# Performance work log

Measured on AMD Instinct MI355X. Metric: run time of the kernel, lower is better.

Reference implementation:

```python
import jax, jax.numpy as jnp
import numpy as np

N_NODES = 100000
HIDDEN = 64
N_EDGES = 1600000


def _sage_conv(x, edge_index, Wl, Wr, b):
    # PyG SAGEConv (mean aggr): out_i = W_l @ mean_{j->i} x_j + W_r @ x_i + b
    src, dst = edge_index[0], edge_index[1]
    msg = x[src]                                      # [E, H] gather
    agg = jax.ops.segment_sum(msg, dst, num_segments=N_NODES)  # [N, H]
    deg = jax.ops.segment_sum(jnp.ones((msg.shape[0],), x.dtype), dst,
                              num_segments=N_NODES)
    agg = agg / jnp.maximum(deg, 1.0)[:, None]
    return agg @ Wl.T + x @ Wr.T + b


def setup_inputs() -> dict:
    key = jax.random.key(0)
    ks = jax.random.split(key, 8)
    s = 1.0 / np.sqrt(HIDDEN)
    return {
        "emb": jax.random.normal(ks[0], (N_NODES, HIDDEN), jnp.float32),
        "Wl1": jax.random.normal(ks[1], (HIDDEN, HIDDEN), jnp.float32) * s,
        "Wr1": jax.random.normal(ks[2], (HIDDEN, HIDDEN), jnp.float32) * s,
        "b1": jnp.zeros((HIDDEN,), jnp.float32),
        "Wl2": jax.random.normal(ks[3], (HIDDEN, HIDDEN), jnp.float32) * s,
        "Wr2": jax.random.normal(ks[4], (HIDDEN, HIDDEN), jnp.float32) * s,
        "b2": jnp.zeros((HIDDEN,), jnp.float32),
        "node_id": jnp.arange(N_NODES, dtype=jnp.int64 if jax.config.jax_enable_x64 else jnp.int32),
        "edge_index": jax.random.randint(ks[5], (2, N_EDGES), 0, N_NODES),
    }


def reference(emb, Wl1, Wr1, b1, Wl2, Wr2, b2, node_id, edge_index):
    # Embedding lookup
    x = emb[node_id]                                   # [N, H]
    # GNN: relu(conv1) -> conv2
    x = jax.nn.relu(_sage_conv(x, edge_index, Wl1, Wr1, b1))
    x = _sage_conv(x, edge_index, Wl2, Wr2, b2)
    # Classifier: per-edge dot product of endpoint features
    ef1 = x[edge_index[0]]                             # [E, H]
    ef2 = x[edge_index[1]]                             # [E, H]
    return (ef1 * ef2).sum(axis=-1)                    # [E]
```

## Files before the change

### kernel.cpp

```cpp
#include <hip/hip_runtime.h>

#define N_NODES 100000
#define HID 64
#define N_EDGES 1600000
#define NB 391
#define C_EPB 6400

typedef __attribute__((ext_vector_type(8))) short bf16x8;
typedef __attribute__((ext_vector_type(4))) float f32x4;

__device__ __forceinline__ unsigned short f2bf(float f) {
    unsigned u = __float_as_uint(f);
    u = (u + 0x7FFFu + ((u >> 16) & 1u)) >> 16;
    return (unsigned short)u;
}
__device__ __forceinline__ float bf2f(unsigned short h) {
    return __uint_as_float(((unsigned)h) << 16);
}
__device__ __forceinline__ float bflo(unsigned w) { return __uint_as_float(w << 16); }
__device__ __forceinline__ float bfhi(unsigned w) { return __uint_as_float(w & 0xFFFF0000u); }

__global__ void gather_bf16_kernel(const float* __restrict__ emb,
                                   const int* __restrict__ nid,
                                   unsigned short* __restrict__ xh) {
    int i = blockIdx.x * blockDim.x + threadIdx.x;
    const int total = N_NODES * (HID / 4);
    if (i >= total) return;
    int row = i >> 4;
    int c   = i & 15;
    int s   = nid[row];
    float4 v = reinterpret_cast<const float4*>(emb)[(size_t)s * 16 + c];
    uint2 p;
    p.x = (unsigned)f2bf(v.x) | ((unsigned)f2bf(v.y) << 16);
    p.y = (unsigned)f2bf(v.z) | ((unsigned)f2bf(v.w) << 16);
    reinterpret_cast<uint2*>(xh)[(size_t)row * 16 + c] = p;
}

__global__ void bucket_hist(const int* __restrict__ dst,
                            int* __restrict__ bhist) {
    __shared__ int h[NB];
    for (int i = threadIdx.x; i < NB; i += blockDim.x) h[i] = 0;
    __syncthreads();
    int nt = gridDim.x * blockDim.x;
    const int4* d4 = (const int4*)dst;
    for (int q = blockIdx.x * blockDim.x + threadIdx.x; q < N_EDGES / 4; q += nt) {
        int4 v = d4[q];
        atomicAdd(&h[v.x >> 8], 1);
        atomicAdd(&h[v.y >> 8], 1);
        atomicAdd(&h[v.z >> 8], 1);
        atomicAdd(&h[v.w >> 8], 1);
    }
    __syncthreads();
    for (int i = threadIdx.x; i < NB; i += blockDim.x)
        if (h[i]) atomicAdd(&bhist[i], h[i]);
}

__global__ void bucket_scan(const int* __restrict__ bhist,
                            int* __restrict__ boff,
                            int* __restrict__ bcursor) {
    __shared__ int s[512];
    int v = (threadIdx.x < NB) ? bhist[threadIdx.x] : 0;
    s[threadIdx.x] = v;
    __syncthreads();
    for (int off = 1; off < 512; off <<= 1) {
        int t = (threadIdx.x >= off) ? s[threadIdx.x - off] : 0;
        __syncthreads();
        s[threadIdx.x] += t;
        __syncthreads();
    }
    if (threadIdx.x < NB) {
        int ex = s[threadIdx.x] - v;
        boff[threadIdx.x] = ex;
        bcursor[threadIdx.x] = ex;
    }
}

__global__ void bucket_scatter(const int* __restrict__ src,
                               const int* __restrict__ dst,
                               int* __restrict__ bcursor,
                               int2* __restrict__ pairs) {
    __shared__ int h[NB];
    __shared__ int base[NB];
    for (int i = threadIdx.x; i < NB; i += blockDim.x) h[i] = 0;
    __syncthreads();
    int e0 = blockIdx.x * C_EPB;
    int e1 = e0 + C_EPB; if (e1 > N_EDGES) e1 = N_EDGES;
    for (int e = e0 + threadIdx.x; e < e1; e += blockDim.x)
        atomicAdd(&h[dst[e] >> 8], 1);
    __syncthreads();
    for (int i = threadIdx.x; i < NB; i += blockDim.x) {
        int c = h[i];
        base[i] = c ? atomicAdd(&bcursor[i], c) : 0;
    }
    __syncthreads();
    for (int i = threadIdx.x; i < NB; i += blockDim.x) h[i] = 0;
    __syncthreads();
    for (int e = e0 + threadIdx.x; e < e1; e += blockDim.x) {
        int d = dst[e];
        int b = d >> 8;
        int slot = base[b] + atomicAdd(&h[b], 1);
        pairs[slot] = make_int2(src[e], d);
    }
}

__global__ void bucket_csr(const int2* __restrict__ pairs,
                           const int* __restrict__ boff,
                           const int* __restrict__ bcursor,
                           int* __restrict__ row_start,
                           int* __restrict__ adj) {
    __shared__ int cnt[256];
    __shared__ int sc[256];
    int b = blockIdx.x;
    int node0 = b << 8;
    int p0 = boff[b];
    int p1 = bcursor[b];
    int t = threadIdx.x;
    cnt[t] = 0;
    __syncthreads();
    for (int p = p0 + t; p < p1; p += 256)
        atomicAdd(&cnt[pairs[p].y & 255], 1);
    __syncthreads();
    int v = cnt[t];
    sc[t] = v;
    __syncthreads();
    for (int off = 1; off < 256; off <<= 1) {
        int u = (t >= off) ? sc[t - off] : 0;
        __syncthreads();
        sc[t] += u;
        __syncthreads();
    }
    sc[t] = p0 + sc[t] - v;
    __syncthreads();
    int node = node0 + t;
    if (node <= N_NODES) row_start[node] = sc[t];
    __syncthreads();
    for (int p = p0 + t; p < p1; p += 256) {
        int2 pr = pairs[p];
        int slot = atomicAdd(&sc[pr.y & 255], 1);
        adj[slot] = pr.x;
    }
}

__global__ void agg_kernel(const int* __restrict__ row_start,
                           const int* __restrict__ adj,
                           const unsigned short* __restrict__ xh,
                           unsigned short* __restrict__ M) {
    int lane = threadIdx.x & 63;
    int slot = lane >> 4;
    int c    = lane & 15;
    int wpb = blockDim.x >> 6;
    int wid = blockIdx.x * wpb + (threadIdx.x >> 6);
    int stride = gridDim.x * wpb;
    const uint2* xw = (const uint2*)xh;
    uint2* Mw = (uint2*)M;
    for (int row = wid; row < N_NODES; row += stride) {
        int beg = row_start[row], end = row_start[row + 1];
        float a0 = 0.f, a1 = 0.f, a2 = 0.f, a3 = 0.f;
        int j = beg + slot;
        for (; j + 12 < end; j += 16) {
            int s0 = adj[j], s1 = adj[j + 4], s2 = adj[j + 8], s3 = adj[j + 12];
            uint2 v0 = xw[(size_t)s0 * 16 + c];
            uint2 v1 = xw[(size_t)s1 * 16 + c];
            uint2 v2 = xw[(size_t)s2 * 16 + c];
            uint2 v3 = xw[(size_t)s3 * 16 + c];
            a0 += bflo(v0.x) + bflo(v1.x) + bflo(v2.x) + bflo(v3.x);
            a1 += bfhi(v0.x) + bfhi(v1.x) + bfhi(v2.x) + bfhi(v3.x);
            a2 += bflo(v0.y) + bflo(v1.y) + bflo(v2.y) + bflo(v3.y);
            a3 += bfhi(v0.y) + bfhi(v1.y) + bfhi(v2.y) + bfhi(v3.y);
        }
        for (; j < end; j += 4) {
            uint2 v = xw[(size_t)adj[j] * 16 + c];
            a0 += bflo(v.x); a1 += bfhi(v.x);
            a2 += bflo(v.y); a3 += bfhi(v.y);
        }
        a0 += __shfl_xor(a0, 16); a0 += __shfl_xor(a0, 32);
        a1 += __shfl_xor(a1, 16); a1 += __shfl_xor(a1, 32);
        a2 += __shfl_xor(a2, 16); a2 += __shfl_xor(a2, 32);
        a3 += __shfl_xor(a3, 16); a3 += __shfl_xor(a3, 32);
        if (slot == 0) {
            float inv = 1.0f / fmaxf((float)(end - beg), 1.0f);
            uint2 p;
            p.x = (unsigned)f2bf(a0 * inv) | ((unsigned)f2bf(a1 * inv) << 16);
            p.y = (unsigned)f2bf(a2 * inv) | ((unsigned)f2bf(a3 * inv) << 16);
            Mw[(size_t)row * 16 + c] = p;
        }
    }
}

__global__ void gemm_kernel(const unsigned short* __restrict__ Am,
                            const unsigned short* __restrict__ As,
                            const float* __restrict__ Wl,
                            const float* __restrict__ Wr,
                            const float* __restrict__ bias,
                            unsigned short* __restrict__ H,
                            int relu) {
    int lane = threadIdx.x & 63;
    int m = lane & 15, quad = lane >> 4;

    bf16x8 wf[2][2][4];
    for (int mat = 0; mat < 2; ++mat) {
        const float* W = mat ? Wr : Wl;
        for (int ks = 0; ks < 2; ++ks)
            for (int ct = 0; ct < 4; ++ct) {
                const float* p = W + (ct * 16 + m) * HID + ks * 32 + quad * 8;
                bf16x8 f;
                #pragma unroll
                for (int j = 0; j < 8; ++j) f[j] = (short)f2bf(p[j]);
                wf[mat][ks][ct] = f;
            }
    }
    float bv[4];
    #pragma unroll
    for (int ct = 0; ct < 4; ++ct) bv[ct] = bias[ct * 16 + m];

    int wpb = blockDim.x >> 6;
    int wid = blockIdx.x * wpb + (threadIdx.x >> 6);
    int stride = gridDim.x * wpb;
    const int NT = N_NODES / 16;
    for (int t = wid; t < NT; t += stride) {
        f32x4 acc[4] = {{0,0,0,0},{0,0,0,0},{0,0,0,0},{0,0,0,0}};
        size_t rowbase = ((size_t)t * 16 + m) * HID;
        #pragma unroll
        for (int ks = 0; ks < 2; ++ks) {
            bf16x8 a0 = *(const bf16x8*)(Am + rowbase + ks * 32 + quad * 8);
            bf16x8 a1 = *(const bf16x8*)(As + rowbase + ks * 32 + quad * 8);
            #pragma unroll
            for (int ct = 0; ct < 4; ++ct) {
                acc[ct] = __builtin_amdgcn_mfma_f32_16x16x32_bf16(a0, wf[0][ks][ct], acc[ct], 0, 0, 0);
                acc[ct] = __builtin_amdgcn_mfma_f32_16x16x32_bf16(a1, wf[1][ks][ct], acc[ct], 0, 0, 0);
            }
        }
        #pragma unroll
        for (int ct = 0; ct < 4; ++ct) {
            #pragma unroll
            for (int r = 0; r < 4; ++r) {
                float v = acc[ct][r] + bv[ct];
                if (relu) v = fmaxf(v, 0.f);
                H[((size_t)t * 16 + quad * 4 + r) * HID + ct * 16 + m] = f2bf(v);
            }
        }
    }
}

__global__ void edge_dot_kernel(const int* __restrict__ src,
                                const int* __restrict__ dst,
                                const unsigned short* __restrict__ h,
                                float* __restrict__ out) {
    int t = blockIdx.x * blockDim.x + threadIdx.x;
    int g = t >> 3;
    int c = t & 7;
    int e0 = g * 2;
    if (e0 >= N_EDGES) return;
    int a0 = src[e0],     b0 = dst[e0];
    int a1 = src[e0 + 1], b1 = dst[e0 + 1];
    const uint4* h4 = reinterpret_cast<const uint4*>(h);
    uint4 va0 = h4[(size_t)a0 * 8 + c];
    uint4 vb0 = h4[(size_t)b0 * 8 + c];
    uint4 va1 = h4[(size_t)a1 * 8 + c];
    uint4 vb1 = h4[(size_t)b1 * 8 + c];
    float p0 = bflo(va0.x) * bflo(vb0.x) + bfhi(va0.x) * bfhi(vb0.x)
             + bflo(va0.y) * bflo(vb0.y) + bfhi(va0.y) * bfhi(vb0.y)
             + bflo(va0.z) * bflo(vb0.z) + bfhi(va0.z) * bfhi(vb0.z)
             + bflo(va0.w) * bflo(vb0.w) + bfhi(va0.w) * bfhi(vb0.w);
    float p1 = bflo(va1.x) * bflo(vb1.x) + bfhi(va1.x) * bfhi(vb1.x)
             + bflo(va1.y) * bflo(vb1.y) + bfhi(va1.y) * bfhi(vb1.y)
             + bflo(va1.z) * bflo(vb1.z) + bfhi(va1.z) * bfhi(vb1.z)
             + bflo(va1.w) * bflo(vb1.w) + bfhi(va1.w) * bfhi(vb1.w);
    p0 += __shfl_xor(p0, 1); p0 += __shfl_xor(p0, 2); p0 += __shfl_xor(p0, 4);
    p1 += __shfl_xor(p1, 1); p1 += __shfl_xor(p1, 2); p1 += __shfl_xor(p1, 4);
    if (c == 0) reinterpret_cast<float2*>(out)[g] = make_float2(p0, p1);
}

extern "C" void kernel_launch(void* const* d_in, const int* in_sizes, int n_in,
                              void* d_out, int out_size, void* d_ws, size_t ws_size,
                              hipStream_t stream) {
    const float* emb = (const float*)d_in[0];
    const float* Wl1 = (const float*)d_in[1];
    const float* Wr1 = (const float*)d_in[2];
    const float* b1  = (const float*)d_in[3];
    const float* Wl2 = (const float*)d_in[4];
    const float* Wr2 = (const float*)d_in[5];
    const float* b2  = (const float*)d_in[6];
    const int*   nid = (const int*)d_in[7];
    const int*   ei  = (const int*)d_in[8];
    const int* esrc = ei;
    const int* edst = ei + N_EDGES;
    float* out = (float*)d_out;

    const size_t NH = (size_t)N_NODES * HID;
    unsigned short* xh  = (unsigned short*)d_ws;
    unsigned short* h1h = xh + NH;
    unsigned short* h2h = h1h + NH;
    unsigned short* M   = h2h + NH;
    int* ib        = (int*)(M + NH);
    int* row_start = ib;
    int* adj       = ib + N_NODES + 64;
    int2* pairs    = (int2*)(adj + N_EDGES + 64);
    int* bhist     = (int*)(pairs + N_EDGES);
    int* boff      = bhist + NB + 1;
    int* bcursor   = boff + NB + 1;

    hipMemsetAsync(bhist, 0, NB * sizeof(int), stream);

    gather_bf16_kernel<<<(N_NODES * 16 + 255) / 256, 256, 0, stream>>>(emb, nid, xh);

    bucket_hist<<<256, 256, 0, stream>>>(edst, bhist);
    bucket_scan<<<1, 512, 0, stream>>>(bhist, boff, bcursor);
    bucket_scatter<<<(N_EDGES + C_EPB - 1) / C_EPB, 256, 0, stream>>>(esrc, edst, bcursor, pairs);
    bucket_csr<<<NB, 256, 0, stream>>>(pairs, boff, bcursor, row_start, adj);

    agg_kernel<<<2048, 256, 0, stream>>>(row_start, adj, xh, M);
    gemm_kernel<<<512, 256, 0, stream>>>(M, xh, Wl1, Wr1, b1, h1h, 1);

    agg_kernel<<<2048, 256, 0, stream>>>(row_start, adj, h1h, M);
    gemm_kernel<<<512, 256, 0, stream>>>(M, h1h, Wl2, Wr2, b2, h2h, 0);

    edge_dot_kernel<<<((size_t)(N_EDGES / 2) * 8 + 255) / 256, 256, 0, stream>>>(esrc, edst, h2h, out);
}
```

Before: 304.3 us.

## Fuse neighbor aggregation into SAGE GEMM and merge gather with histogram

Neighbor mean aggregation now happens inside the MFMA GEMM kernel. Each lane walks one row's adjacency list and builds the aggregated bf16 fragment in registers, so the intermediate M buffer is never written and re-read. The embedding gather and bucket histogram are merged into one launch, and bucket_scatter reads src/dst as int4. The cost is a different aggregation mapping: one lane per row walking edges serially, with 16 accumulators per lane. That may lower memory-level parallelism and cause load imbalance across rows of different degree.

```diff
diff --git a/kernel.cpp b/kernel.cpp
--- a/kernel.cpp
+++ b/kernel.cpp
@@ -5,6 +5,7 @@
 #define N_EDGES 1600000
 #define NB 391
 #define C_EPB 6400
+#define G_GATHER 6250
 
 typedef __attribute__((ext_vector_type(8))) short bf16x8;
 typedef __attribute__((ext_vector_type(4))) float f32x4;
@@ -14,45 +15,49 @@
     u = (u + 0x7FFFu + ((u >> 16) & 1u)) >> 16;
     return (unsigned short)u;
 }
-__device__ __forceinline__ float bf2f(unsigned short h) {
-    return __uint_as_float(((unsigned)h) << 16);
-}
 __device__ __forceinline__ float bflo(unsigned w) { return __uint_as_float(w << 16); }
 __device__ __forceinline__ float bfhi(unsigned w) { return __uint_as_float(w & 0xFFFF0000u); }
 
-__global__ void gather_bf16_kernel(const float* __restrict__ emb,
+__device__ __forceinline__ void acc8(float* a, uint4 u) {
+    a[0] += bflo(u.x); a[1] += bfhi(u.x);
+    a[2] += bflo(u.y); a[3] += bfhi(u.y);
+    a[4] += bflo(u.z); a[5] += bfhi(u.z);
+    a[6] += bflo(u.w); a[7] += bfhi(u.w);
+}
+
+__global__ void gather_hist_kernel(const float* __restrict__ emb,
                                    const int* __restrict__ nid,
-                                   unsigned short* __restrict__ xh) {
-    int i = blockIdx.x * blockDim.x + threadIdx.x;
-    const int total = N_NODES * (HID / 4);
-    if (i >= total) return;
-    int row = i >> 4;
-    int c   = i & 15;
-    int s   = nid[row];
-    float4 v = reinterpret_cast<const float4*>(emb)[(size_t)s * 16 + c];
-    uint2 p;
-    p.x = (unsigned)f2bf(v.x) | ((unsigned)f2bf(v.y) << 16);
-    p.y = (unsigned)f2bf(v.z) | ((unsigned)f2bf(v.w) << 16);
-    reinterpret_cast<uint2*>(xh)[(size_t)row * 16 + c] = p;
-}
-
-__global__ void bucket_hist(const int* __restrict__ dst,
-                            int* __restrict__ bhist) {
+                                   unsigned short* __restrict__ xh,
+                                   const int* __restrict__ dst,
+                                   int* __restrict__ bhist) {
     __shared__ int h[NB];
-    for (int i = threadIdx.x; i < NB; i += blockDim.x) h[i] = 0;
-    __syncthreads();
-    int nt = gridDim.x * blockDim.x;
-    const int4* d4 = (const int4*)dst;
-    for (int q = blockIdx.x * blockDim.x + threadIdx.x; q < N_EDGES / 4; q += nt) {
-        int4 v = d4[q];
-        atomicAdd(&h[v.x >> 8], 1);
-        atomicAdd(&h[v.y >> 8], 1);
-        atomicAdd(&h[v.z >> 8], 1);
-        atomicAdd(&h[v.w >> 8], 1);
-    }
-    __syncthreads();
-    for (int i = threadIdx.x; i < NB; i += blockDim.x)
-        if (h[i]) atomicAdd(&bhist[i], h[i]);
+    if (blockIdx.x < G_GATHER) {
+        int i = blockIdx.x * blockDim.x + threadIdx.x;
+        int row = i >> 4;
+        int c   = i & 15;
+        int s   = nid[row];
+        float4 v = reinterpret_cast<const float4*>(emb)[(size_t)s * 16 + c];
+        uint2 p;
+        p.x = (unsigned)f2bf(v.x) | ((unsigned)f2bf(v.y) << 16);
+        p.y = (unsigned)f2bf(v.z) | ((unsigned)f2bf(v.w) << 16);
+        reinterpret_cast<uint2*>(xh)[(size_t)row * 16 + c] = p;
+    } else {
+        int hb = blockIdx.x - G_GATHER;
+        for (int i = threadIdx.x; i < NB; i += blockDim.x) h[i] = 0;
+        __syncthreads();
+        int nt = 256 * blockDim.x;
+        const int4* d4 = (const int4*)dst;
+        for (int q = hb * blockDim.x + threadIdx.x; q < N_EDGES / 4; q += nt) {
+            int4 v = d4[q];
+            atomicAdd(&h[v.x >> 8], 1);
+            atomicAdd(&h[v.y >> 8], 1);
+            atomicAdd(&h[v.z >> 8], 1);
+            atomicAdd(&h[v.w >> 8], 1);
+        }
+        __syncthreads();
+        for (int i = threadIdx.x; i < NB; i += blockDim.x)
+            if (h[i]) atomicAdd(&bhist[i], h[i]);
+    }
 }
 
 __global__ void bucket_scan(const int* __restrict__ bhist,
@@ -83,10 +88,17 @@
     __shared__ int base[NB];
     for (int i = threadIdx.x; i < NB; i += blockDim.x) h[i] = 0;
     __syncthreads();
-    int e0 = blockIdx.x * C_EPB;
-    int e1 = e0 + C_EPB; if (e1 > N_EDGES) e1 = N_EDGES;
-    for (int e = e0 + threadIdx.x; e < e1; e += blockDim.x)
-        atomicAdd(&h[dst[e] >> 8], 1);
+    int q0 = blockIdx.x * (C_EPB / 4);
+    int q1 = q0 + (C_EPB / 4);
+    const int4* d4 = (const int4*)dst;
+    const int4* s4 = (const int4*)src;
+    for (int q = q0 + threadIdx.x; q < q1; q += blockDim.x) {
+        int4 v = d4[q];
+        atomicAdd(&h[v.x >> 8], 1);
+        atomicAdd(&h[v.y >> 8], 1);
+        atomicAdd(&h[v.z >> 8], 1);
+        atomicAdd(&h[v.w >> 8], 1);
+    }
     __syncthreads();
     for (int i = threadIdx.x; i < NB; i += blockDim.x) {
         int c = h[i];
@@ -95,11 +107,14 @@
     __syncthreads();
     for (int i = threadIdx.x; i < NB; i += blockDim.x) h[i] = 0;
     __syncthreads();
-    for (int e = e0 + threadIdx.x; e < e1; e += blockDim.x) {
-        int d = dst[e];
-        int b = d >> 8;
-        int slot = base[b] + atomicAdd(&h[b], 1);
-        pairs[slot] = make_int2(src[e], d);
+    for (int q = q0 + threadIdx.x; q < q1; q += blockDim.x) {
+        int4 d = d4[q];
+        int4 s = s4[q];
+        int b, slot;
+        b = d.x >> 8; slot = base[b] + atomicAdd(&h[b], 1); pairs[slot] = make_int2(s.x, d.x);
+        b = d.y >> 8; slot = base[b] + atomicAdd(&h[b], 1); pairs[slot] = make_int2(s.y, d.y);
+        b = d.z >> 8; slot = base[b] + atomicAdd(&h[b], 1); pairs[slot] = make_int2(s.z, d.z);
+        b = d.w >> 8; slot = base[b] + atomicAdd(&h[b], 1); pairs[slot] = make_int2(s.w, d.w);
     }
 }
 
@@ -141,59 +156,14 @@
     }
 }
 
-__global__ void agg_kernel(const int* __restrict__ row_start,
+__global__ void sage_fused(const int* __restrict__ row_start,
                            const int* __restrict__ adj,
                            const unsigned short* __restrict__ xh,
-                           unsigned short* __restrict__ M) {
-    int lane = threadIdx.x & 63;
-    int slot = lane >> 4;
-    int c    = lane & 15;
-    int wpb = blockDim.x >> 6;
-    int wid = blockIdx.x * wpb + (threadIdx.x >> 6);
-    int stride = gridDim.x * wpb;
-    const uint2* xw = (const uint2*)xh;
-    uint2* Mw = (uint2*)M;
-    for (int row = wid; row < N_NODES; row += stride) {
-        int beg = row_start[row], end = row_start[row + 1];
-        float a0 = 0.f, a1 = 0.f, a2 = 0.f, a3 = 0.f;
-        int j = beg + slot;
-        for (; j + 12 < end; j += 16) {
-            int s0 = adj[j], s1 = adj[j + 4], s2 = adj[j + 8], s3 = adj[j + 12];
-            uint2 v0 = xw[(size_t)s0 * 16 + c];
-            uint2 v1 = xw[(size_t)s1 * 16 + c];
-            uint2 v2 = xw[(size_t)s2 * 16 + c];
-            uint2 v3 = xw[(size_t)s3 * 16 + c];
-            a0 += bflo(v0.x) + bflo(v1.x) + bflo(v2.x) + bflo(v3.x);
-            a1 += bfhi(v0.x) + bfhi(v1.x) + bfhi(v2.x) + bfhi(v3.x);
-            a2 += bflo(v0.y) + bflo(v1.y) + bflo(v2.y) + bflo(v3.y);
-            a3 += bfhi(v0.y) + bfhi(v1.y) + bfhi(v2.y) + bfhi(v3.y);
-        }
-        for (; j < end; j += 4) {
-            uint2 v = xw[(size_t)adj[j] * 16 + c];
-            a0 += bflo(v.x); a1 += bfhi(v.x);
-            a2 += bflo(v.y); a3 += bfhi(v.y);
-        }
-        a0 += __shfl_xor(a0, 16); a0 += __shfl_xor(a0, 32);
-        a1 += __shfl_xor(a1, 16); a1 += __shfl_xor(a1, 32);
-        a2 += __shfl_xor(a2, 16); a2 += __shfl_xor(a2, 32);
-        a3 += __shfl_xor(a3, 16); a3 += __shfl_xor(a3, 32);
-        if (slot == 0) {
-            float inv = 1.0f / fmaxf((float)(end - beg), 1.0f);
-            uint2 p;
-            p.x = (unsigned)f2bf(a0 * inv) | ((unsigned)f2bf(a1 * inv) << 16);
-            p.y = (unsigned)f2bf(a2 * inv) | ((unsigned)f2bf(a3 * inv) << 16);
-            Mw[(size_t)row * 16 + c] = p;
-        }
-    }
-}
-
-__global__ void gemm_kernel(const unsigned short* __restrict__ Am,
-                            const unsigned short* __restrict__ As,
-                            const float* __restrict__ Wl,
-                            const float* __restrict__ Wr,
-                            const float* __restrict__ bias,
-                            unsigned short* __restrict__ H,
-                            int relu) {
+                           const float* __restrict__ Wl,
+                           const float* __restrict__ Wr,
+                           const float* __restrict__ bias,
+                           unsigned short* __restrict__ H,
+                           int relu) {
     int lane = threadIdx.x & 63;
     int m = lane & 15, quad = lane >> 4;
 
@@ -217,18 +187,54 @@
     int wid = blockIdx.x * wpb + (threadIdx.x >> 6);
     int stride = gridDim.x * wpb;
     const int NT = N_NODES / 16;
+    const uint4* x4 = (const uint4*)xh;
+
     for (int t = wid; t < NT; t += stride) {
+        int row = t * 16 + m;
+        int beg = row_start[row], end = row_start[row + 1];
+        float ag[16];
+        #pragma unroll
+        for (int i = 0; i < 16; ++i) ag[i] = 0.f;
+
+        int j = beg;
+        for (; j + 3 < end; j += 4) {
+            int s0 = adj[j], s1 = adj[j + 1], s2 = adj[j + 2], s3 = adj[j + 3];
+            uint4 a0 = x4[(size_t)s0 * 8 + quad];
+            uint4 b0 = x4[(size_t)s0 * 8 + 4 + quad];
+            uint4 a1 = x4[(size_t)s1 * 8 + quad];
+            uint4 b1 = x4[(size_t)s1 * 8 + 4 + quad];
+            uint4 a2 = x4[(size_t)s2 * 8 + quad];
+            uint4 b2 = x4[(size_t)s2 * 8 + 4 + quad];
+            uint4 a3 = x4[(size_t)s3 * 8 + quad];
+            uint4 b3 = x4[(size_t)s3 * 8 + 4 + quad];
+            acc8(ag, a0); acc8(ag + 8, b0);
+            acc8(ag, a1); acc8(ag + 8, b1);
+            acc8(ag, a2); acc8(ag + 8, b2);
+            acc8(ag, a3); acc8(ag + 8, b3);
+        }
+        for (; j < end; ++j) {
+            int s = adj[j];
+            acc8(ag,     x4[(size_t)s * 8 + quad]);
+            acc8(ag + 8, x4[(size_t)s * 8 + 4 + quad]);
+        }
+
+        float inv = 1.0f / fmaxf((float)(end - beg), 1.0f);
+        bf16x8 am0, am1, as0, as1;
+        #pragma unroll
+        for (int i = 0; i < 8; ++i) {
+            am0[i] = (short)f2bf(ag[i] * inv);
+            am1[i] = (short)f2bf(ag[8 + i] * inv);
+        }
+        as0 = *(const bf16x8*)(xh + (size_t)row * HID + quad * 8);
+        as1 = *(const bf16x8*)(xh + (size_t)row * HID + 32 + quad * 8);
+
         f32x4 acc[4] = {{0,0,0,0},{0,0,0,0},{0,0,0,0},{0,0,0,0}};
-        size_t rowbase = ((size_t)t * 16 + m) * HID;
         #pragma unroll
-        for (int ks = 0; ks < 2; ++ks) {
-            bf16x8 a0 = *(const bf16x8*)(Am + rowbase + ks * 32 + quad * 8);
-            bf16x8 a1 = *(const bf16x8*)(As + rowbase + ks * 32 + quad * 8);
-            #pragma unroll
-            for (int ct = 0; ct < 4; ++ct) {
-                acc[ct] = __builtin_amdgcn_mfma_f32_16x16x32_bf16(a0, wf[0][ks][ct], acc[ct], 0, 0, 0);
-                acc[ct] = __builtin_amdgcn_mfma_f32_16x16x32_bf16(a1, wf[1][ks][ct], acc[ct], 0, 0, 0);
-            }
+        for (int ct = 0; ct < 4; ++ct) {
+            acc[ct] = __builtin_amdgcn_mfma_f32_16x16x32_bf16(am0, wf[0][0][ct], acc[ct], 0, 0, 0);
+            acc[ct] = __builtin_amdgcn_mfma_f32_16x16x32_bf16(am1, wf[0][1][ct], acc[ct], 0, 0, 0);
+            acc[ct] = __builtin_amdgcn_mfma_f32_16x16x32_bf16(as0, wf[1][0][ct], acc[ct], 0, 0, 0);
+            acc[ct] = __builtin_amdgcn_mfma_f32_16x16x32_bf16(as1, wf[1][1][ct], acc[ct], 0, 0, 0);
         }
         #pragma unroll
         for (int ct = 0; ct < 4; ++ct) {
@@ -291,8 +297,7 @@
     unsigned short* xh  = (unsigned short*)d_ws;
     unsigned short* h1h = xh + NH;
     unsigned short* h2h = h1h + NH;
-    unsigned short* M   = h2h + NH;
-    int* ib        = (int*)(M + NH);
+    int* ib        = (int*)(h2h + NH);
     int* row_start = ib;
     int* adj       = ib + N_NODES + 64;
     int2* pairs    = (int2*)(adj + N_EDGES + 64);
@@ -302,18 +307,14 @@
 
     hipMemsetAsync(bhist, 0, NB * sizeof(int), stream);
 
-    gather_bf16_kernel<<<(N_NODES * 16 + 255) / 256, 256, 0, stream>>>(emb, nid, xh);
-
-    bucket_hist<<<256, 256, 0, stream>>>(edst, bhist);
+    gather_hist_kernel<<<G_GATHER + 256, 256, 0, stream>>>(emb, nid, xh, edst, bhist);
+
     bucket_scan<<<1, 512, 0, stream>>>(bhist, boff, bcursor);
-    bucket_scatter<<<(N_EDGES + C_EPB - 1) / C_EPB, 256, 0, stream>>>(esrc, edst, bcursor, pairs);
+    bucket_scatter<<<N_EDGES / C_EPB, 256, 0, stream>>>(esrc, edst, bcursor, pairs);
     bucket_csr<<<NB, 256, 0, stream>>>(pairs, boff, bcursor, row_start, adj);
 
-    agg_kernel<<<2048, 256, 0, stream>>>(row_start, adj, xh, M);
-    gemm_kernel<<<512, 256, 0, stream>>>(M, xh, Wl1, Wr1, b1, h1h, 1);
-
-    agg_kernel<<<2048, 256, 0, stream>>>(row_start, adj, h1h, M);
-    gemm_kernel<<<512, 256, 0, stream>>>(M, h1h, Wl2, Wr2, b2, h2h, 0);
+    sage_fused<<<1024, 256, 0, stream>>>(row_start, adj, xh,  Wl1, Wr1, b1, h1h, 1);
+    sage_fused<<<1024, 256, 0, stream>>>(row_start, adj, h1h, Wl2, Wr2, b2, h2h, 0);
 
     edge_dot_kernel<<<((size_t)(N_EDGES / 2) * 8 + 255) / 256, 256, 0, stream>>>(esrc, edst, h2h, out);
 }
```

New measurement: 312.8 us. 1.03x slower.
